# Optimization experiments

Hardware: AMD Instinct MI355X
Metric: run time of the kernel (lower is better)

Reference implementation:

```python
import jax, jax.numpy as jnp
import numpy as np

D_MODEL = 512
NUM_HEADS = 8
HEAD_DIM = D_MODEL // NUM_HEADS
EPS = 1e-6


def setup_inputs() -> dict:
    key = jax.random.key(0)
    ks = jax.random.split(key, 9)
    s = 1.0 / np.sqrt(D_MODEL)
    x = jax.random.normal(ks[0], (4, 8192, D_MODEL), dtype=jnp.float32)
    Wq = jax.random.uniform(ks[1], (D_MODEL, D_MODEL), jnp.float32, -s, s)
    bq = jax.random.uniform(ks[2], (D_MODEL,), jnp.float32, -s, s)
    Wk = jax.random.uniform(ks[3], (D_MODEL, D_MODEL), jnp.float32, -s, s)
    bk = jax.random.uniform(ks[4], (D_MODEL,), jnp.float32, -s, s)
    Wv = jax.random.uniform(ks[5], (D_MODEL, D_MODEL), jnp.float32, -s, s)
    bv = jax.random.uniform(ks[6], (D_MODEL,), jnp.float32, -s, s)
    Wo = jax.random.uniform(ks[7], (D_MODEL, D_MODEL), jnp.float32, -s, s)
    bo = jax.random.uniform(ks[8], (D_MODEL,), jnp.float32, -s, s)
    return {"x": x, "Wq": Wq, "bq": bq, "Wk": Wk, "bk": bk,
            "Wv": Wv, "bv": bv, "Wo": Wo, "bo": bo}


def _feature_map(t):
    # ELU(x) + 1
    return jax.nn.elu(t) + 1.0


def reference(x, Wq, bq, Wk, bk, Wv, bv, Wo, bo):
    B, N, C = x.shape
    H, D = NUM_HEADS, HEAD_DIM
    # projections: torch Linear computes x @ W.T + b
    q = (x @ Wq.T + bq).reshape(B, N, H, D).transpose(0, 2, 1, 3)  # [B,H,N,D]
    k = (x @ Wk.T + bk).reshape(B, N, H, D).transpose(0, 2, 1, 3)
    v = (x @ Wv.T + bv).reshape(B, N, H, D).transpose(0, 2, 1, 3)
    q = _feature_map(q)
    k = _feature_map(k)
    # kv: [B,H,D,D] = k^T v   (global, non-causal linear attention)
    kv = jnp.einsum('bhnd,bhne->bhde', k, v)
    # normalizer: q . sum_n(k)  -> [B,H,N,1]
    k_sum = k.sum(axis=2)  # [B,H,D]
    z = jnp.einsum('bhnd,bhd->bhn', q, k_sum)[..., None] + EPS
    out = jnp.einsum('bhnd,bhde->bhne', q, kv) / z  # [B,H,N,D]
    out = out.transpose(0, 2, 1, 3).reshape(B, N, C)
    return out @ Wo.T + bo
```

## Files before the change

### kernel.cpp

```cpp
#include <hip/hip_runtime.h>
#include <hip/hip_bf16.h>

typedef __attribute__((ext_vector_type(8))) short short8;
typedef __attribute__((ext_vector_type(4))) float f32x4;
typedef unsigned short u16;
typedef unsigned int u32;

#define T_TOK 32768
#define CDIM  512
#define HEADS 8
#define HD    64
#define NSEQ  8192

__device__ __forceinline__ u16 f2bf(float f) {
  u32 u = __builtin_bit_cast(u32, f);
  u = u + 0x7fffu + ((u >> 16) & 1u);
  return (u16)(u >> 16);
}
__device__ __forceinline__ float bf2f(u16 s) {
  return __builtin_bit_cast(float, ((u32)s) << 16);
}

__global__ __launch_bounds__(256) void k_convx(const float* __restrict__ x,
                                               u16* __restrict__ xb) {
  size_t i = (size_t)blockIdx.x * 256 + threadIdx.x;
  size_t stride = (size_t)gridDim.x * 256;
  size_t total = (size_t)T_TOK * 512 / 8;
  for (; i < total; i += stride) {
    float4 a = *reinterpret_cast<const float4*>(&x[i * 8]);
    float4 b = *reinterpret_cast<const float4*>(&x[i * 8 + 4]);
    ushort4 r0, r1;
    r0.x = f2bf(a.x); r0.y = f2bf(a.y); r0.z = f2bf(a.z); r0.w = f2bf(a.w);
    r1.x = f2bf(b.x); r1.y = f2bf(b.y); r1.z = f2bf(b.z); r1.w = f2bf(b.w);
    *reinterpret_cast<ushort4*>(&xb[i * 8])     = r0;
    *reinterpret_cast<ushort4*>(&xb[i * 8 + 4]) = r1;
  }
}

__global__ void k_pack_w(const float* __restrict__ Wq, const float* __restrict__ Wk,
                         const float* __restrict__ Wv, const float* __restrict__ Wo,
                         u16* __restrict__ Wcat) {
  int idx = blockIdx.x * 256 + threadIdx.x;
  int c = idx & 511;
  int o2 = idx >> 9;
  const float* W = (o2 < 512) ? Wq : (o2 < 1024) ? Wk : (o2 < 1536) ? Wv : Wo;
  int o = o2 & 511;
  Wcat[idx] = f2bf(W[o * 512 + c]);
}

template<int MODE>
__global__ __launch_bounds__(512, 2) void k_gemm(const u16* __restrict__ Ag,
    const u16* __restrict__ Wcat,
    const float* __restrict__ b0, const float* __restrict__ b1, const float* __restrict__ b2,
    u16* __restrict__ obf, float* __restrict__ of32) {
  constexpr int NT = (MODE == 0) ? 6 : 2;
  constexpr int BROW = (MODE == 0) ? 0 : 1536;
  constexpr int OSTRIDE = (MODE == 0) ? 1536 : 512;
  __shared__ u16 As[2][256][64];
  __shared__ u16 Bs[2][256][64];
  int bid = blockIdx.x;
  constexpr int GRID = (T_TOK / 256) * NT;
  constexpr int CHUNK = GRID / 8;
  int swz = (bid & 7) * CHUNK + (bid >> 3);
  int m0 = (swz / NT) * 256;
  int n0 = (swz % NT) * 256;
  int tid = threadIdx.x;
  int lane = tid & 63, w = tid >> 6;
  int wr = w >> 2, wc = w & 3;
  f32x4 acc_a[4][4], acc_b[4][4];
  _Pragma("unroll")
  for (int i = 0; i < 4; ++i)
    _Pragma("unroll")
    for (int j = 0; j < 4; ++j) { acc_a[i][j] = (f32x4)0.0f; acc_b[i][j] = (f32x4)0.0f; }

  const u16* Bg = Wcat + (size_t)BROW * 512;
  int grl = lane >> 3;
  int gcl = (((lane & 7) ^ grl)) * 8;
  int l15 = lane & 15, lhi = lane >> 4, sx = lane & 7;

#define STAGE(buf, k0)                                                                     \
  _Pragma("unroll")                                                                        \
  for (int i = 0; i < 4; ++i) {                                                            \
    int r = i * 64 + w * 8;                                                                \
    __builtin_amdgcn_global_load_lds(                                                      \
        (const __attribute__((address_space(1))) void*)&Ag[(size_t)(m0 + r + grl) * 512 + (k0) + gcl], \
        (__attribute__((address_space(3))) void*)&As[buf][r][0], 16, 0, 0);                \
    __builtin_amdgcn_global_load_lds(                                                      \
        (const __attribute__((address_space(1))) void*)&Bg[(size_t)(n0 + r + grl) * 512 + (k0) + gcl], \
        (__attribute__((address_space(3))) void*)&Bs[buf][r][0], 16, 0, 0);                \
  }

#define COMPUTE(buf)                                                                       \
  _Pragma("unroll")                                                                        \
  for (int kk = 0; kk < 2; ++kk) {                                                         \
    int slot = (kk * 4 + lhi) ^ sx;                                                        \
    short8 bfr[4];                                                                         \
    _Pragma("unroll")                                                                      \
    for (int n = 0; n < 4; ++n)                                                            \
      bfr[n] = *reinterpret_cast<const short8*>(&Bs[buf][wc * 64 + n * 16 + l15][slot * 8]);\
    {                                                                                      \
      short8 af[4];                                                                        \
      _Pragma("unroll")                                                                    \
      for (int m = 0; m < 4; ++m)                                                          \
        af[m] = *reinterpret_cast<const short8*>(&As[buf][wr * 128 + m * 16 + l15][slot * 8]); \
      _Pragma("unroll")                                                                    \
      for (int m = 0; m < 4; ++m)                                                          \
        _Pragma("unroll")                                                                  \
        for (int n = 0; n < 4; ++n)                                                        \
          acc_a[m][n] = __builtin_amdgcn_mfma_f32_16x16x32_bf16(af[m], bfr[n], acc_a[m][n], 0, 0, 0); \
    }                                                                                      \
    {                                                                                      \
      short8 af[4];                                                                        \
      _Pragma("unroll")                                                                    \
      for (int m = 0; m < 4; ++m)                                                          \
        af[m] = *reinterpret_cast<const short8*>(&As[buf][wr * 128 + 64 + m * 16 + l15][slot * 8]); \
      _Pragma("unroll")                                                                    \
      for (int m = 0; m < 4; ++m)                                                          \
        _Pragma("unroll")                                                                  \
        for (int n = 0; n < 4; ++n)                                                        \
          acc_b[m][n] = __builtin_amdgcn_mfma_f32_16x16x32_bf16(af[m], bfr[n], acc_b[m][n], 0, 0, 0); \
    }                                                                                      \
  }

  STAGE(0, 0)
  __syncthreads();
  int cur = 0;
  for (int t = 0; t < 7; ++t) {
    STAGE(cur ^ 1, (t + 1) * 64)
    COMPUTE(cur)
    __syncthreads();
    cur ^= 1;
  }
  COMPUTE(cur)
#undef STAGE
#undef COMPUTE

  _Pragma("unroll")
  for (int m = 0; m < 4; ++m) {
    _Pragma("unroll")
    for (int half = 0; half < 2; ++half) {
      int row = m0 + wr * 128 + half * 64 + m * 16 + lhi * 4;
      _Pragma("unroll")
      for (int n = 0; n < 4; ++n) {
        int col = n0 + wc * 64 + n * 16 + l15;
        float bias;
        if (MODE == 0)
          bias = (col < 512) ? b0[col] : (col < 1024) ? b1[col - 512] : b2[col - 1024];
        else
          bias = b0[col];
        _Pragma("unroll")
        for (int j = 0; j < 4; ++j) {
          float vv = (half == 0 ? acc_a[m][n][j] : acc_b[m][n][j]) + bias;
          if (MODE == 0) {
            if (col < 1024) vv = (vv > 0.0f) ? (vv + 1.0f) : __expf(vv);
            obf[(size_t)(row + j) * OSTRIDE + col] = f2bf(vv);
          } else {
            of32[(size_t)(row + j) * OSTRIDE + col] = vv;
          }
        }
      }
    }
  }
}

__global__ __launch_bounds__(256) void k_kvstats(const u16* __restrict__ qkv,
    float* __restrict__ kvp, float* __restrict__ ksp) {
  __shared__ u16 kt[64][32];
  __shared__ u16 vt[64][32];
  __shared__ float ks_red[4][64];
  int hh = blockIdx.x;
  int s  = blockIdx.y;
  int b = hh >> 3, h = hh & 7;
  int tid = threadIdx.x;
  int lane = tid & 63, w = tid >> 6;
  size_t tbase = (size_t)b * NSEQ + (size_t)s * 512;
  f32x4 acc[4];
  for (int n = 0; n < 4; ++n) acc[n] = (f32x4)0.0f;
  float ksum_loc = 0.0f;
  int kcol = 512 + h * 64;
  int vcol = 1024 + h * 64;
  int l15 = lane & 15;
  int rsw = 8 * (l15 >> 2);

  for (int step = 0; step < 16; ++step) {
    size_t t0 = tbase + (size_t)step * 32;
    for (int jj = 0; jj < 4; ++jj) {
      int id = tid + 256 * jj;
      int trow = (id >> 4) & 31;
      int dq = id & 15;
      int isv = id >> 9;
      ushort4 val = *reinterpret_cast<const ushort4*>(
          &qkv[(t0 + trow) * 1536 + (isv ? vcol : kcol) + dq * 4]);
      u16 (*dst)[32] = isv ? vt : kt;
      int colw = trow ^ (8 * (dq & 3));
      dst[dq * 4 + 0][colw] = val.x;
      dst[dq * 4 + 1][colw] = val.y;
      dst[dq * 4 + 2][colw] = val.z;
      dst[dq * 4 + 3][colw] = val.w;
    }
    __syncthreads();
    {
      int d = tid & 63, g = tid >> 6;
      int gs = 8 * (g ^ ((d >> 2) & 3));
      float sl = 0;
      for (int i = 0; i < 8; ++i) sl += bf2f(kt[d][gs + i]);
      ksum_loc += sl;
    }
    int kb = 8 * (lane >> 4);
    short8 af = *reinterpret_cast<const short8*>(&kt[w * 16 + l15][kb ^ rsw]);
    for (int n = 0; n < 4; ++n) {
      short8 bfr = *reinterpret_cast<const short8*>(&vt[n * 16 + l15][kb ^ rsw]);
      acc[n] = __builtin_amdgcn_mfma_f32_16x16x32_bf16(af, bfr, acc[n], 0, 0, 0);
    }
    __syncthreads();
  }
  size_t pbase = ((size_t)hh * 16 + s) * 4096;
  for (int n = 0; n < 4; ++n) {
    int d = w * 16 + (lane >> 4) * 4;
    int e = n * 16 + (lane & 15);
    for (int j = 0; j < 4; ++j)
      kvp[pbase + (size_t)(d + j) * 64 + e] = acc[n][j];
  }
  ks_red[tid >> 6][tid & 63] = ksum_loc;
  __syncthreads();
  if (tid < 64) {
    float r = ks_red[0][tid] + ks_red[1][tid] + ks_red[2][tid] + ks_red[3][tid];
    ksp[((size_t)hh * 16 + s) * 64 + tid] = r;
  }
}

__global__ void k_reduce(const float* __restrict__ kvp, const float* __restrict__ ksp,
                         u16* __restrict__ kvb, float* __restrict__ ksum) {
  int hh = blockIdx.x;
  int tid = threadIdx.x;
  for (int j = 0; j < 16; ++j) {
    int idx = tid + 256 * j;
    float a = 0;
    for (int s = 0; s < 16; ++s) a += kvp[((size_t)hh * 16 + s) * 4096 + idx];
    int d = idx >> 6, e = idx & 63;
    kvb[(size_t)hh * 4096 + e * 64 + d] = f2bf(a);
  }
  if (tid < 64) {
    float a = 0;
    for (int s = 0; s < 16; ++s) a += ksp[((size_t)hh * 16 + s) * 64 + tid];
    ksum[hh * 64 + tid] = a;
  }
}

__global__ __launch_bounds__(256) void k_attn(const u16* __restrict__ qkv,
    const u16* __restrict__ kvb, const float* __restrict__ ksum,
    u16* __restrict__ attn) {
  __shared__ u16 qf[32][520];
  __shared__ float zl[32][8];
  __shared__ float kss[8][64];
  int tid = threadIdx.x;
  int lane = tid & 63, w = tid >> 6;
  size_t t0 = (size_t)blockIdx.x * 32;
  int b = (int)(t0 >> 13);
  for (int jj = 0; jj < 16; ++jj) {
    int id = tid + 256 * jj;
    int row = id >> 7, cq = id & 127;
    *reinterpret_cast<ushort4*>(&qf[row][cq * 4]) =
        *reinterpret_cast<const ushort4*>(&qkv[(t0 + row) * 1536 + cq * 4]);
  }
  { int i = tid, i2 = tid + 256;
    kss[i >> 6][i & 63]   = ksum[b * 512 + i];
    kss[i2 >> 6][i2 & 63] = ksum[b * 512 + i2]; }
  __syncthreads();
  {
    int tok = tid & 31, h = tid >> 5;
    float z = 0;
    for (int jq = 0; jq < 8; ++jq) {
      short8 qv = *reinterpret_cast<const short8*>(&qf[tok][h * 64 + jq * 8]);
      for (int e = 0; e < 8; ++e) z += bf2f((u16)qv[e]) * kss[h][jq * 8 + e];
    }
    zl[tok][h] = z + 1e-6f;
  }
  __syncthreads();
  for (int hi = 0; hi < 2; ++hi) {
    int h = w * 2 + hi;
    size_t kvoff = (size_t)(b * 8 + h) * 4096;
    f32x4 acc[2][4];
    for (int m = 0; m < 2; ++m) for (int n = 0; n < 4; ++n) acc[m][n] = (f32x4)0.0f;
    for (int kk = 0; kk < 2; ++kk) {
      int kb = kk * 32 + 8 * (lane >> 4);
      short8 af[2], bfr[4];
      for (int m = 0; m < 2; ++m)
        af[m] = *reinterpret_cast<const short8*>(&qf[m * 16 + (lane & 15)][h * 64 + kb]);
      for (int n = 0; n < 4; ++n)
        bfr[n] = *reinterpret_cast<const short8*>(&kvb[kvoff + (size_t)(n * 16 + (lane & 15)) * 64 + kb]);
      for (int m = 0; m < 2; ++m)
        for (int n = 0; n < 4; ++n)
          acc[m][n] = __builtin_amdgcn_mfma_f32_16x16x32_bf16(af[m], bfr[n], acc[m][n], 0, 0, 0);
    }
    for (int m = 0; m < 2; ++m) {
      int tokb = m * 16 + (lane >> 4) * 4;
      for (int n = 0; n < 4; ++n) {
        int e = n * 16 + (lane & 15);
        for (int j = 0; j < 4; ++j) {
          float vv = acc[m][n][j] / zl[tokb + j][h];
          attn[(t0 + tokb + j) * 512 + h * 64 + e] = f2bf(vv);
        }
      }
    }
  }
}

extern "C" void kernel_launch(void* const* d_in, const int* in_sizes, int n_in,
                              void* d_out, int out_size, void* d_ws, size_t ws_size,
                              hipStream_t stream) {
  const float* x  = (const float*)d_in[0];
  const float* Wq = (const float*)d_in[1];
  const float* bq = (const float*)d_in[2];
  const float* Wk = (const float*)d_in[3];
  const float* bk = (const float*)d_in[4];
  const float* Wv = (const float*)d_in[5];
  const float* bv = (const float*)d_in[6];
  const float* Wo = (const float*)d_in[7];
  const float* bo = (const float*)d_in[8];
  float* out = (float*)d_out;

  char* ws = (char*)d_ws;
  u16*   Wcat = (u16*)(ws + 0);
  u16*   qkv  = (u16*)(ws + 2097152);
  u16*   xb   = (u16*)(ws + 102760448);
  float* kvp  = (float*)(ws + 102760448);
  u16*   attn = (u16*)(ws + 102760448);
  float* ksp  = (float*)(ws + 136314880);
  u16*   kvb  = (u16*)(ws + 136445952);
  float* ksum = (float*)(ws + 136708096);

  k_convx  <<<2048, 256, 0, stream>>>(x, xb);
  k_pack_w <<<4096, 256, 0, stream>>>(Wq, Wk, Wv, Wo, Wcat);
  k_gemm<0><<<768, 512, 0, stream>>>(xb, Wcat, bq, bk, bv, qkv, nullptr);
  k_kvstats<<<dim3(32, 16), 256, 0, stream>>>(qkv, kvp, ksp);
  k_reduce <<<32, 256, 0, stream>>>(kvp, ksp, kvb, ksum);
  k_attn   <<<1024, 256, 0, stream>>>(qkv, kvb, ksum, attn);
  k_gemm<1><<<256, 512, 0, stream>>>(attn, Wcat, bo, nullptr, nullptr, nullptr, out);
}
```

Baseline: 177.7 us.

## Deepen GEMM prefetch pipeline with vmcnt waits, MFMA priority, and parallelize reduce

The GEMM main loop now issues two stages ahead and waits with explicit s_waitcnt vmcnt counts plus raw barriers instead of __syncthreads. This lets the next tile's global-to-LDS loads overlap the MFMA work rather than draining all memory traffic at every step. MFMA blocks are wrapped in s_setprio so the math wave gets issue priority. The k_reduce kernel is split across 8 slices per head (256 blocks instead of 32) to expose more parallelism. The vmcnt(8) value depends on the exact number of loads STAGE emits, so a wrong count could introduce a race.

```diff
diff --git a/kernel.cpp b/kernel.cpp
--- a/kernel.cpp
+++ b/kernel.cpp
@@ -103,35 +103,46 @@
       _Pragma("unroll")                                                                    \
       for (int m = 0; m < 4; ++m)                                                          \
         af[m] = *reinterpret_cast<const short8*>(&As[buf][wr * 128 + m * 16 + l15][slot * 8]); \
+      __builtin_amdgcn_s_setprio(1);                                                       \
       _Pragma("unroll")                                                                    \
       for (int m = 0; m < 4; ++m)                                                          \
         _Pragma("unroll")                                                                  \
         for (int n = 0; n < 4; ++n)                                                        \
           acc_a[m][n] = __builtin_amdgcn_mfma_f32_16x16x32_bf16(af[m], bfr[n], acc_a[m][n], 0, 0, 0); \
+      __builtin_amdgcn_s_setprio(0);                                                       \
     }                                                                                      \
     {                                                                                      \
       short8 af[4];                                                                        \
       _Pragma("unroll")                                                                    \
       for (int m = 0; m < 4; ++m)                                                          \
         af[m] = *reinterpret_cast<const short8*>(&As[buf][wr * 128 + 64 + m * 16 + l15][slot * 8]); \
+      __builtin_amdgcn_s_setprio(1);                                                       \
       _Pragma("unroll")                                                                    \
       for (int m = 0; m < 4; ++m)                                                          \
         _Pragma("unroll")                                                                  \
         for (int n = 0; n < 4; ++n)                                                        \
           acc_b[m][n] = __builtin_amdgcn_mfma_f32_16x16x32_bf16(af[m], bfr[n], acc_b[m][n], 0, 0, 0); \
+      __builtin_amdgcn_s_setprio(0);                                                       \
     }                                                                                      \
   }
 
   STAGE(0, 0)
-  __syncthreads();
-  int cur = 0;
+  STAGE(1, 64)
+  asm volatile("s_waitcnt vmcnt(8)" ::: "memory");
+  __builtin_amdgcn_s_barrier();
+  _Pragma("unroll")
   for (int t = 0; t < 7; ++t) {
-    STAGE(cur ^ 1, (t + 1) * 64)
-    COMPUTE(cur)
-    __syncthreads();
-    cur ^= 1;
-  }
-  COMPUTE(cur)
+    COMPUTE(t & 1)
+    __builtin_amdgcn_s_barrier();
+    if (t < 6) {
+      STAGE(t & 1, (t + 2) * 64)
+      asm volatile("s_waitcnt vmcnt(8)" ::: "memory");
+    } else {
+      asm volatile("s_waitcnt vmcnt(0)" ::: "memory");
+    }
+    __builtin_amdgcn_s_barrier();
+  }
+  COMPUTE(1)
 #undef STAGE
 #undef COMPUTE
 
@@ -232,15 +243,16 @@
 __global__ void k_reduce(const float* __restrict__ kvp, const float* __restrict__ ksp,
                          u16* __restrict__ kvb, float* __restrict__ ksum) {
   int hh = blockIdx.x;
+  int sl = blockIdx.y;
   int tid = threadIdx.x;
-  for (int j = 0; j < 16; ++j) {
-    int idx = tid + 256 * j;
+  for (int j = 0; j < 2; ++j) {
+    int idx = sl * 512 + tid + 256 * j;
     float a = 0;
     for (int s = 0; s < 16; ++s) a += kvp[((size_t)hh * 16 + s) * 4096 + idx];
     int d = idx >> 6, e = idx & 63;
     kvb[(size_t)hh * 4096 + e * 64 + d] = f2bf(a);
   }
-  if (tid < 64) {
+  if (sl == 0 && tid < 64) {
     float a = 0;
     for (int s = 0; s < 16; ++s) a += ksp[((size_t)hh * 16 + s) * 64 + tid];
     ksum[hh * 64 + tid] = a;
@@ -334,7 +346,7 @@
   k_pack_w <<<4096, 256, 0, stream>>>(Wq, Wk, Wv, Wo, Wcat);
   k_gemm<0><<<768, 512, 0, stream>>>(xb, Wcat, bq, bk, bv, qkv, nullptr);
   k_kvstats<<<dim3(32, 16), 256, 0, stream>>>(qkv, kvp, ksp);
-  k_reduce <<<32, 256, 0, stream>>>(kvp, ksp, kvb, ksum);
+  k_reduce <<<dim3(32, 8), 256, 0, stream>>>(kvp, ksp, kvb, ksum);
   k_attn   <<<1024, 256, 0, stream>>>(qkv, kvb, ksum, attn);
   k_gemm<1><<<256, 512, 0, stream>>>(attn, Wcat, bo, nullptr, nullptr, nullptr, out);
 }
```

Measured after the change: 171.8 us. 1.03x faster.
